# Kernel tuning notes

Hardware: AMD Instinct MI355X
Metric: run time of the kernel (lower is better)

Reference implementation:

```python
import jax, jax.numpy as jnp
import numpy as np

NEG_SLOPE = 0.2  # PyG GATConv default negative_slope


def _gat_layer(x, src, dst, n_nodes, W, a_src, a_dst, b):
    # x: [N, din]; src/dst: [E] (self-loops already included)
    h = x @ W                                  # [N, dout]
    s_src = h @ a_src                          # [N]
    s_dst = h @ a_dst                          # [N]
    e = jax.nn.leaky_relu(s_src[src] + s_dst[dst], NEG_SLOPE)  # [E]
    # per-target-node softmax over incoming edges (stable via segment max)
    m = jax.ops.segment_max(e, dst, num_segments=n_nodes)      # [N]
    a = jnp.exp(e - m[dst])                    # [E]
    denom = jax.ops.segment_sum(a, dst, num_segments=n_nodes)  # [N]
    msg = h[src] * a[:, None]                  # [E, dout]
    agg = jax.ops.segment_sum(msg, dst, num_segments=n_nodes)  # [N, dout]
    return agg / denom[:, None] + b


def setup_inputs() -> dict:
    key = jax.random.key(0)
    ks = jax.random.split(key, 16)
    N, E = 100000, 1600000
    in_dim, hid_dim, out_dim = 128, 128, 64
    x = jax.random.normal(ks[0], (N, in_dim), dtype=jnp.float32)
    edge_idx = jax.random.randint(ks[1], (2, E), 0, N, dtype=jnp.int32)

    def lin(k, din, dout):
        return jax.random.normal(k, (din, dout), dtype=jnp.float32) * (1.0 / np.sqrt(din))

    def att(k, dout):
        return jax.random.normal(k, (dout,), dtype=jnp.float32) * (1.0 / np.sqrt(dout))

    return {
        "x": x, "edge_idx": edge_idx,
        "W1": lin(ks[2], in_dim, hid_dim), "as1": att(ks[3], hid_dim), "ad1": att(ks[4], hid_dim), "b1": jnp.zeros((hid_dim,), jnp.float32),
        "W2": lin(ks[5], hid_dim, hid_dim), "as2": att(ks[6], hid_dim), "ad2": att(ks[7], hid_dim), "b2": jnp.zeros((hid_dim,), jnp.float32),
        "W3": lin(ks[8], hid_dim, out_dim), "as3": att(ks[9], out_dim), "ad3": att(ks[10], out_dim), "b3": jnp.zeros((out_dim,), jnp.float32),
    }


def reference(x, edge_idx, W1, as1, ad1, b1, W2, as2, ad2, b2, W3, as3, ad3, b3):
    N = x.shape[0]
    # add self-loops (PyG GATConv default add_self_loops=True)
    loops = jnp.arange(N, dtype=edge_idx.dtype)
    src = jnp.concatenate([edge_idx[0], loops])
    dst = jnp.concatenate([edge_idx[1], loops])
    h = _gat_layer(x, src, dst, N, W1, as1, ad1, b1)
    h = _gat_layer(h, src, dst, N, W2, as2, ad2, b2)
    h = _gat_layer(h, src, dst, N, W3, as3, ad3, b3)
    return jnp.mean(h, axis=-2)  # [out_dim]
```

## Files before the change

kernel.cpp:

```cpp
#include <hip/hip_runtime.h>

static inline int ceil_div(long long a, long long b) { return (int)((a + b - 1) / b); }

typedef __attribute__((ext_vector_type(8))) short bf16x8;
typedef __attribute__((ext_vector_type(4))) float f32x4;

__device__ __forceinline__ float lrelu(float t) { return t > 0.f ? t : 0.2f * t; }

__device__ __forceinline__ void atomAddF(float* p, float v) {
  unsafeAtomicAdd(p, v);
}

__device__ __forceinline__ unsigned int f2bf(float f) {
  unsigned int u = __float_as_uint(f);
  unsigned int r = ((u >> 16) & 1u) + 0x7fffu;
  return (u + r) >> 16;
}

__global__ void cvt_bf16(const float* __restrict__ X, unsigned short* __restrict__ Xb, int n4) {
  int i = blockIdx.x * blockDim.x + threadIdx.x;
  if (i < n4) {
    const float4 v = ((const float4*)X)[i];
    uint2 o;
    o.x = f2bf(v.x) | (f2bf(v.y) << 16);
    o.y = f2bf(v.z) | (f2bf(v.w) << 16);
    ((uint2*)Xb)[i] = o;
  }
}

__global__ void transpose_w(const float* __restrict__ W, unsigned short* __restrict__ Wt,
                            int DINv, int DOUTv) {
  int idx = blockIdx.x * blockDim.x + threadIdx.x;
  if (idx < DINv * DOUTv) {
    int k = idx / DOUTv, n = idx % DOUTv;
    Wt[n * DINv + k] = (unsigned short)f2bf(W[idx]);
  }
}

template<int DOUT>
__launch_bounds__(256)
__global__ void gemm_mfma(const unsigned short* __restrict__ Xb, const unsigned short* __restrict__ Wt,
                          const float* __restrict__ avs, const float* __restrict__ avd,
                          unsigned short* __restrict__ Hb, float* __restrict__ Ss,
                          float* __restrict__ Sd, int N, int RG) {
  constexpr int DIN = 128;
  constexpr int CG = DOUT / 64;
  const int wave = (int)((blockIdx.x * (unsigned)blockDim.x + threadIdx.x) >> 6);
  const int rg = wave / CG;
  const int cg = wave % CG;
  if (rg >= RG) return;
  const int lane = threadIdx.x & 63;
  const int l16 = lane & 15, quad = lane >> 4;
  const int row0 = rg * 64, colw0 = cg * 64;

  int xoff[4], woff[4];
#pragma unroll
  for (int t = 0; t < 4; t++) {
    int m = row0 + t * 16 + l16; if (m > N - 1) m = N - 1;
    xoff[t] = m * DIN + quad * 8;
    woff[t] = (colw0 + t * 16 + l16) * DIN + quad * 8;
  }

  f32x4 acc[4][4];
#pragma unroll
  for (int a = 0; a < 4; a++)
#pragma unroll
    for (int c = 0; c < 4; c++) acc[a][c] = (f32x4)0.f;

#pragma unroll
  for (int kk = 0; kk < 4; kk++) {
    bf16x8 aw[4], bx[4];
#pragma unroll
    for (int t = 0; t < 4; t++) aw[t] = *(const bf16x8*)(Wt + woff[t] + kk * 32);
#pragma unroll
    for (int t = 0; t < 4; t++) bx[t] = *(const bf16x8*)(Xb + xoff[t] + kk * 32);
#pragma unroll
    for (int wt = 0; wt < 4; wt++)
#pragma unroll
      for (int xt = 0; xt < 4; xt++)
        acc[wt][xt] = __builtin_amdgcn_mfma_f32_16x16x32_bf16(aw[wt], bx[xt], acc[wt][xt], 0, 0, 0);
  }

  float4 af[4], df[4];
#pragma unroll
  for (int wt = 0; wt < 4; wt++) {
    af[wt] = *(const float4*)(avs + colw0 + wt * 16 + quad * 4);
    df[wt] = *(const float4*)(avd + colw0 + wt * 16 + quad * 4);
  }
#pragma unroll
  for (int xt = 0; xt < 4; xt++) {
    const int m = row0 + xt * 16 + l16;
    float ps = 0.f, pd = 0.f;
#pragma unroll
    for (int wt = 0; wt < 4; wt++) {
      const f32x4 c = acc[wt][xt];
      ps += c[0]*af[wt].x + c[1]*af[wt].y + c[2]*af[wt].z + c[3]*af[wt].w;
      pd += c[0]*df[wt].x + c[1]*df[wt].y + c[2]*df[wt].z + c[3]*df[wt].w;
    }
    ps += __shfl_xor(ps, 16); ps += __shfl_xor(ps, 32);
    pd += __shfl_xor(pd, 16); pd += __shfl_xor(pd, 32);
    if (quad == 0 && m < N) { atomAddF(&Ss[m], ps); atomAddF(&Sd[m], pd); }
    if (m < N) {
      unsigned short* hp = Hb + (size_t)m * DOUT + colw0 + quad * 4;
#pragma unroll
      for (int wt = 0; wt < 4; wt++) {
        const f32x4 c = acc[wt][xt];
        uint2 o;
        o.x = f2bf(c[0]) | (f2bf(c[1]) << 16);
        o.y = f2bf(c[2]) | (f2bf(c[3]) << 16);
        *(uint2*)(hp + wt * 16) = o;
      }
    }
  }
}

__global__ void hist_rank(const int* __restrict__ dstv, int* __restrict__ cnt,
                          int* __restrict__ rank, int E) {
  int i = blockIdx.x * blockDim.x + threadIdx.x;
  if (i < E) rank[i] = atomicAdd(&cnt[dstv[i]], 1);
}

__global__ void scan_p1(const int* __restrict__ cnt, int* __restrict__ bsum, int N) {
  __shared__ int sm[256];
  const int b = blockIdx.x;
  int s = 0;
  for (int i = threadIdx.x; i < 1024; i += 256) {
    int idx = b * 1024 + i;
    s += (idx < N) ? cnt[idx] : 0;
  }
  sm[threadIdx.x] = s; __syncthreads();
  for (int off = 128; off; off >>= 1) {
    if (threadIdx.x < off) sm[threadIdx.x] += sm[threadIdx.x + off];
    __syncthreads();
  }
  if (threadIdx.x == 0) bsum[b] = sm[0];
}

__global__ void scan_p2(const int* __restrict__ bsum, int* __restrict__ bofs,
                        int NB, int* __restrict__ rowptr_N, int E) {
  __shared__ int sm[1024];
  const int t = threadIdx.x;
  const int v0 = (t < NB) ? bsum[t] : 0;
  sm[t] = v0; __syncthreads();
  for (int off = 1; off < 1024; off <<= 1) {
    int v = (t >= off) ? sm[t - off] : 0;
    __syncthreads();
    sm[t] += v;
    __syncthreads();
  }
  if (t < NB) bofs[t] = sm[t] - v0;
  if (t == 0) *rowptr_N = E;
}

__global__ void scan_p3(const int* __restrict__ cnt, const int* __restrict__ bofs,
                        int* __restrict__ rowptr, int N) {
  __shared__ int sm[1024];
  const int t = threadIdx.x;
  const int idx = blockIdx.x * 1024 + t;
  const int v = (idx < N) ? cnt[idx] : 0;
  sm[t] = v; __syncthreads();
  for (int off = 1; off < 1024; off <<= 1) {
    int u = (t >= off) ? sm[t - off] : 0;
    __syncthreads();
    sm[t] += u;
    __syncthreads();
  }
  if (idx < N) rowptr[idx] = sm[t] - v + bofs[blockIdx.x];
}

__global__ void scatter_k(const int* __restrict__ src, const int* __restrict__ dstv,
                          const int* __restrict__ rank, const int* __restrict__ rowptr,
                          int* __restrict__ srcs, int E) {
  int i = blockIdx.x * blockDim.x + threadIdx.x;
  if (i < E) srcs[rowptr[dstv[i]] + rank[i]] = src[i];
}

template<int DOUT, bool OBF>
__launch_bounds__(256)
__global__ void node_gather(const int* __restrict__ rowptr, const int* __restrict__ srcs,
                            const float* __restrict__ Ss, const float* __restrict__ Sd,
                            const unsigned short* __restrict__ Hb, const float* __restrict__ b,
                            float* __restrict__ out, unsigned short* __restrict__ outb, int N) {
  constexpr int EPL = DOUT / 16;
  constexpr int CAP = 64;
  __shared__ uint2 swL[16][CAP];

  const int l16 = threadIdx.x & 15;
  const int grp = threadIdx.x >> 4;
  const int node = blockIdx.x * 16 + grp;
  if (node >= N) return;

  const int r0 = rowptr[node], r1 = rowptr[node + 1];
  const int deg = r1 - r0;
  const int degc = min(deg, CAP);
  const float sd = Sd[node];
  const float eself = lrelu(Ss[node] + sd);

  float m = eself;
  for (int j0 = 0; j0 < deg; j0 += 16) {
    const int idx = j0 + l16;
    float e = -1e30f;
    if (idx < deg) {
      const int s = srcs[r0 + idx];
      e = lrelu(Ss[s] + sd);
      if (idx < CAP) swL[grp][idx] = make_uint2((unsigned)s, __float_as_uint(e));
    }
    m = fmaxf(m, e);
  }
#pragma unroll
  for (int off = 8; off; off >>= 1) m = fmaxf(m, __shfl_xor(m, off));

  const float wself = __expf(eself - m);
  float lsum = 0.f;
  for (int j0 = 0; j0 < degc; j0 += 16) {
    const int idx = j0 + l16;
    if (idx < degc) {
      uint2 sw = swL[grp][idx];
      const float w = __expf(__uint_as_float(sw.y) - m);
      sw.y = __float_as_uint(w);
      swL[grp][idx] = sw;
      lsum += w;
    }
  }
  for (int j0 = CAP; j0 < deg; j0 += 16) {
    const int idx = j0 + l16;
    if (idx < deg) {
      const int s = srcs[r0 + idx];
      lsum += __expf(lrelu(Ss[s] + sd) - m);
    }
  }
#pragma unroll
  for (int off = 8; off; off >>= 1) lsum += __shfl_xor(lsum, off);
  const float inv = 1.f / (lsum + wself);
  __syncthreads();

  float acc[EPL];
#pragma unroll
  for (int k = 0; k < EPL; k++) acc[k] = 0.f;

  const size_t colb = (size_t)l16 * EPL;
  int j = 0;
  for (; j + 4 <= degc; j += 4) {
    uint2 sw0 = swL[grp][j], sw1 = swL[grp][j+1], sw2 = swL[grp][j+2], sw3 = swL[grp][j+3];
    const unsigned short* p0 = Hb + (size_t)sw0.x * DOUT + colb;
    const unsigned short* p1 = Hb + (size_t)sw1.x * DOUT + colb;
    const unsigned short* p2 = Hb + (size_t)sw2.x * DOUT + colb;
    const unsigned short* p3 = Hb + (size_t)sw3.x * DOUT + colb;
    if (EPL == 8) {
      const uint4 u0 = *(const uint4*)p0, u1 = *(const uint4*)p1;
      const uint4 u2 = *(const uint4*)p2, u3 = *(const uint4*)p3;
      const float w0 = __uint_as_float(sw0.y), w1 = __uint_as_float(sw1.y);
      const float w2 = __uint_as_float(sw2.y), w3 = __uint_as_float(sw3.y);
      const unsigned int a0[4] = {u0.x,u0.y,u0.z,u0.w}, a1[4] = {u1.x,u1.y,u1.z,u1.w};
      const unsigned int a2[4] = {u2.x,u2.y,u2.z,u2.w}, a3[4] = {u3.x,u3.y,u3.z,u3.w};
#pragma unroll
      for (int k = 0; k < 4; k++) {
        acc[2*k]   += __uint_as_float(a0[k] << 16) * w0 + __uint_as_float(a1[k] << 16) * w1
                    + __uint_as_float(a2[k] << 16) * w2 + __uint_as_float(a3[k] << 16) * w3;
        acc[2*k+1] += __uint_as_float(a0[k] & 0xffff0000u) * w0 + __uint_as_float(a1[k] & 0xffff0000u) * w1
                    + __uint_as_float(a2[k] & 0xffff0000u) * w2 + __uint_as_float(a3[k] & 0xffff0000u) * w3;
      }
    } else {
      const uint2 u0 = *(const uint2*)p0, u1 = *(const uint2*)p1;
      const uint2 u2 = *(const uint2*)p2, u3 = *(const uint2*)p3;
      const float w0 = __uint_as_float(sw0.y), w1 = __uint_as_float(sw1.y);
      const float w2 = __uint_as_float(sw2.y), w3 = __uint_as_float(sw3.y);
      const unsigned int a0[2] = {u0.x,u0.y}, a1[2] = {u1.x,u1.y};
      const unsigned int a2[2] = {u2.x,u2.y}, a3[2] = {u3.x,u3.y};
#pragma unroll
      for (int k = 0; k < 2; k++) {
        acc[2*k]   += __uint_as_float(a0[k] << 16) * w0 + __uint_as_float(a1[k] << 16) * w1
                    + __uint_as_float(a2[k] << 16) * w2 + __uint_as_float(a3[k] << 16) * w3;
        acc[2*k+1] += __uint_as_float(a0[k] & 0xffff0000u) * w0 + __uint_as_float(a1[k] & 0xffff0000u) * w1
                    + __uint_as_float(a2[k] & 0xffff0000u) * w2 + __uint_as_float(a3[k] & 0xffff0000u) * w3;
      }
    }
  }
  for (; j < degc; j++) {
    const uint2 sw = swL[grp][j];
    const float w = __uint_as_float(sw.y);
    const unsigned short* pp = Hb + (size_t)sw.x * DOUT + colb;
#pragma unroll
    for (int k = 0; k < EPL / 2; k++) {
      const unsigned int u = ((const unsigned int*)pp)[k];
      acc[2*k]   += __uint_as_float(u << 16) * w;
      acc[2*k+1] += __uint_as_float(u & 0xffff0000u) * w;
    }
  }
  for (j = CAP; j < deg; j++) {
    const int s = srcs[r0 + j];
    const float w = __expf(lrelu(Ss[s] + sd) - m);
    const unsigned short* pp = Hb + (size_t)s * DOUT + colb;
#pragma unroll
    for (int k = 0; k < EPL / 2; k++) {
      const unsigned int u = ((const unsigned int*)pp)[k];
      acc[2*k]   += __uint_as_float(u << 16) * w;
      acc[2*k+1] += __uint_as_float(u & 0xffff0000u) * w;
    }
  }
  {
    const unsigned short* pp = Hb + (size_t)node * DOUT + colb;
#pragma unroll
    for (int k = 0; k < EPL / 2; k++) {
      const unsigned int u = ((const unsigned int*)pp)[k];
      acc[2*k]   += __uint_as_float(u << 16) * wself;
      acc[2*k+1] += __uint_as_float(u & 0xffff0000u) * wself;
    }
  }

  float o[EPL];
#pragma unroll
  for (int k = 0; k < EPL; k++) o[k] = acc[k] * inv + b[colb + k];
  if (OBF) {
    if (EPL == 8) {
      uint4 u;
      u.x = f2bf(o[0]) | (f2bf(o[1]) << 16);
      u.y = f2bf(o[2]) | (f2bf(o[3]) << 16);
      u.z = f2bf(o[4]) | (f2bf(o[5]) << 16);
      u.w = f2bf(o[6]) | (f2bf(o[7]) << 16);
      *(uint4*)(outb + (size_t)node * DOUT + colb) = u;
    } else {
      uint2 u;
      u.x = f2bf(o[0]) | (f2bf(o[1]) << 16);
      u.y = f2bf(o[2]) | (f2bf(o[3]) << 16);
      *(uint2*)(outb + (size_t)node * DOUT + colb) = u;
    }
  } else {
    float* op = out + (size_t)node * DOUT + colb;
#pragma unroll
    for (int k = 0; k < EPL; k += 4)
      *(float4*)(op + k) = make_float4(o[k], o[k+1], o[k+2], o[k+3]);
  }
}

__global__ void mean64(const float* __restrict__ Hf, float* __restrict__ out, int N, float scale) {
  __shared__ float sm[256];
  const int col = threadIdx.x & 63;
  const int seg = threadIdx.x >> 6;
  const int stride = gridDim.x * 4;
  float s = 0.f;
  for (int n = blockIdx.x * 4 + seg; n < N; n += stride) s += Hf[(size_t)n * 64 + col];
  sm[threadIdx.x] = s;
  __syncthreads();
  if (seg == 0) {
    float tot = sm[col] + sm[64 + col] + sm[128 + col] + sm[192 + col];
    atomAddF(&out[col], tot * scale);
  }
}

extern "C" void kernel_launch(void* const* d_in, const int* in_sizes, int n_in,
                              void* d_out, int out_size, void* d_ws, size_t ws_size,
                              hipStream_t stream) {
  const float* x   = (const float*)d_in[0];
  const int*   ei  = (const int*)d_in[1];
  const float* W1  = (const float*)d_in[2];
  const float* as1 = (const float*)d_in[3];
  const float* ad1 = (const float*)d_in[4];
  const float* b1  = (const float*)d_in[5];
  const float* W2  = (const float*)d_in[6];
  const float* as2 = (const float*)d_in[7];
  const float* ad2 = (const float*)d_in[8];
  const float* b2  = (const float*)d_in[9];
  const float* W3  = (const float*)d_in[10];
  const float* as3 = (const float*)d_in[11];
  const float* ad3 = (const float*)d_in[12];
  const float* b3  = (const float*)d_in[13];

  const int N = in_sizes[0] / 128;
  const int E = in_sizes[1] / 2;
  const int* src  = ei;
  const int* dstv = ei + E;
  const int NB = ceil_div(N, 1024);
  const int RG = ceil_div(N, 64);

  float* p = (float*)d_ws;
  float* bufA = p; p += (size_t)N * 64;
  float* SsSd = p; p += (size_t)2 * N;
  float* Ss = SsSd, *Sd = SsSd + N;
  unsigned short* Xb = (unsigned short*)p; p += (size_t)N * 64;
  unsigned short* Hb = (unsigned short*)p; p += (size_t)N * 64;
  unsigned short* Wt1 = (unsigned short*)p; p += 128 * 128 / 2;
  unsigned short* Wt2 = (unsigned short*)p; p += 128 * 128 / 2;
  unsigned short* Wt3 = (unsigned short*)p; p += 128 * 64 / 2;
  int* ip = (int*)p;
  int* cnt     = ip; ip += N;
  int* rowptr  = ip; ip += N + 1;
  int* bsum    = ip; ip += NB;
  int* bofs    = ip; ip += NB;
  int* rank    = ip; ip += E;
  int* srcs    = ip; ip += E;

  hipMemsetAsync(cnt, 0, (size_t)N * sizeof(int), stream);
  hist_rank<<<ceil_div(E, 256), 256, 0, stream>>>(dstv, cnt, rank, E);
  scan_p1<<<NB, 256, 0, stream>>>(cnt, bsum, N);
  scan_p2<<<1, 1024, 0, stream>>>(bsum, bofs, NB, rowptr + N, E);
  scan_p3<<<NB, 1024, 0, stream>>>(cnt, bofs, rowptr, N);
  scatter_k<<<ceil_div(E, 256), 256, 0, stream>>>(src, dstv, rank, rowptr, srcs, E);

  transpose_w<<<ceil_div(128 * 128, 256), 256, 0, stream>>>(W1, Wt1, 128, 128);
  transpose_w<<<ceil_div(128 * 128, 256), 256, 0, stream>>>(W2, Wt2, 128, 128);
  transpose_w<<<ceil_div(128 * 64, 256), 256, 0, stream>>>(W3, Wt3, 128, 64);
  cvt_bf16<<<ceil_div((long long)N * 32, 256), 256, 0, stream>>>(x, Xb, N * 32);

  const int GG = ceil_div(N, 16);
  hipMemsetAsync(SsSd, 0, (size_t)2 * N * sizeof(float), stream);
  gemm_mfma<128><<<ceil_div((long long)RG * 2, 4), 256, 0, stream>>>(Xb, Wt1, as1, ad1, Hb, Ss, Sd, N, RG);
  node_gather<128, true><<<GG, 256, 0, stream>>>(rowptr, srcs, Ss, Sd, Hb, b1, nullptr, Xb, N);
  hipMemsetAsync(SsSd, 0, (size_t)2 * N * sizeof(float), stream);
  gemm_mfma<128><<<ceil_div((long long)RG * 2, 4), 256, 0, stream>>>(Xb, Wt2, as2, ad2, Hb, Ss, Sd, N, RG);
  node_gather<128, true><<<GG, 256, 0, stream>>>(rowptr, srcs, Ss, Sd, Hb, b2, nullptr, Xb, N);
  hipMemsetAsync(SsSd, 0, (size_t)2 * N * sizeof(float), stream);
  gemm_mfma<64><<<ceil_div((long long)RG, 4), 256, 0, stream>>>(Xb, Wt3, as3, ad3, Hb, Ss, Sd, N, RG);
  node_gather<64, false><<<GG, 256, 0, stream>>>(rowptr, srcs, Ss, Sd, Hb, b3, bufA, nullptr, N);

  hipMemsetAsync(d_out, 0, 64 * sizeof(float), stream);
  mean64<<<256, 256, 0, stream>>>(bufA, (float*)d_out, N, 1.0f / (float)N);
}
```

Baseline: 488.2 us.

## Replace atomic CSR build with two-level bucketed counting sort

```diff
diff --git a/kernel.cpp b/kernel.cpp
--- a/kernel.cpp
+++ b/kernel.cpp
@@ -4,6 +4,9 @@
 
 typedef __attribute__((ext_vector_type(8))) short bf16x8;
 typedef __attribute__((ext_vector_type(4))) float f32x4;
+
+#define TILE 8192
+#define BKSH 9
 
 __device__ __forceinline__ float lrelu(float t) { return t > 0.f ? t : 0.2f * t; }
 
@@ -114,65 +117,103 @@
   }
 }
 
-__global__ void hist_rank(const int* __restrict__ dstv, int* __restrict__ cnt,
-                          int* __restrict__ rank, int E) {
-  int i = blockIdx.x * blockDim.x + threadIdx.x;
-  if (i < E) rank[i] = atomicAdd(&cnt[dstv[i]], 1);
-}
-
-__global__ void scan_p1(const int* __restrict__ cnt, int* __restrict__ bsum, int N) {
-  __shared__ int sm[256];
-  const int b = blockIdx.x;
+__launch_bounds__(256)
+__global__ void bucket_hist(const int* __restrict__ dstv, int* __restrict__ bh,
+                            int E, int NBUK) {
+  __shared__ int h[256];
+  h[threadIdx.x] = 0;
+  __syncthreads();
+  const int base = blockIdx.x * TILE;
+  const int end = min(E, base + TILE);
+  for (int i = base + threadIdx.x; i < end; i += 256)
+    atomicAdd(&h[dstv[i] >> BKSH], 1);
+  __syncthreads();
+  if (threadIdx.x < NBUK) bh[blockIdx.x * NBUK + threadIdx.x] = h[threadIdx.x];
+}
+
+__launch_bounds__(256)
+__global__ void bucket_scan(int* __restrict__ bh, int* __restrict__ bucketBase,
+                            int* __restrict__ rowptr_N, int NBA, int NBUK, int E) {
+  __shared__ int tot[256], sc[256];
+  const int t = threadIdx.x;
   int s = 0;
-  for (int i = threadIdx.x; i < 1024; i += 256) {
-    int idx = b * 1024 + i;
-    s += (idx < N) ? cnt[idx] : 0;
-  }
-  sm[threadIdx.x] = s; __syncthreads();
-  for (int off = 128; off; off >>= 1) {
-    if (threadIdx.x < off) sm[threadIdx.x] += sm[threadIdx.x + off];
+  if (t < NBUK)
+    for (int blk = 0; blk < NBA; blk++) s += bh[blk * NBUK + t];
+  tot[t] = s; sc[t] = s;
+  __syncthreads();
+  for (int off = 1; off < 256; off <<= 1) {
+    int v = (t >= off) ? sc[t - off] : 0;
     __syncthreads();
-  }
-  if (threadIdx.x == 0) bsum[b] = sm[0];
-}
-
-__global__ void scan_p2(const int* __restrict__ bsum, int* __restrict__ bofs,
-                        int NB, int* __restrict__ rowptr_N, int E) {
-  __shared__ int sm[1024];
+    sc[t] += v;
+    __syncthreads();
+  }
+  const int base = sc[t] - tot[t];
+  if (t < NBUK) bucketBase[t] = base;
+  if (t == 0) { bucketBase[NBUK] = E; *rowptr_N = E; }
+  if (t < NBUK) {
+    int run = base;
+    for (int blk = 0; blk < NBA; blk++) {
+      const int c = bh[blk * NBUK + t];
+      bh[blk * NBUK + t] = run;
+      run += c;
+    }
+  }
+}
+
+__launch_bounds__(256)
+__global__ void bucket_scatter(const int* __restrict__ src, const int* __restrict__ dstv,
+                               const int* __restrict__ bh, unsigned int* __restrict__ pairs,
+                               int E, int NBUK) {
+  __shared__ int ofs[256];
+  if (threadIdx.x < NBUK) ofs[threadIdx.x] = bh[blockIdx.x * NBUK + threadIdx.x];
+  __syncthreads();
+  const int base = blockIdx.x * TILE;
+  const int end = min(E, base + TILE);
+  for (int i = base + threadIdx.x; i < end; i += 256) {
+    const int d = dstv[i];
+    const int pos = atomicAdd(&ofs[d >> BKSH], 1);
+    pairs[pos] = ((unsigned int)src[i] << BKSH) | (unsigned int)(d & ((1 << BKSH) - 1));
+  }
+}
+
+__launch_bounds__(256)
+__global__ void region_build(const unsigned int* __restrict__ pairs,
+                             const int* __restrict__ bucketBase,
+                             int* __restrict__ rowptr, int* __restrict__ srcs, int N) {
+  __shared__ int cnt[512], ofs[512], ps[256];
   const int t = threadIdx.x;
-  const int v0 = (t < NB) ? bsum[t] : 0;
-  sm[t] = v0; __syncthreads();
-  for (int off = 1; off < 1024; off <<= 1) {
-    int v = (t >= off) ? sm[t - off] : 0;
+  const int r = blockIdx.x;
+  const int p0 = bucketBase[r], p1 = bucketBase[r + 1];
+  cnt[t] = 0; cnt[t + 256] = 0;
+  __syncthreads();
+  for (int i = p0 + t; i < p1; i += 256)
+    atomicAdd(&cnt[pairs[i] & 511u], 1);
+  __syncthreads();
+  const int c0 = cnt[2 * t], c1 = cnt[2 * t + 1];
+  const int pr = c0 + c1;
+  ps[t] = pr;
+  __syncthreads();
+  for (int off = 1; off < 256; off <<= 1) {
+    int v = (t >= off) ? ps[t - off] : 0;
     __syncthreads();
-    sm[t] += v;
+    ps[t] += v;
     __syncthreads();
   }
-  if (t < NB) bofs[t] = sm[t] - v0;
-  if (t == 0) *rowptr_N = E;
-}
-
-__global__ void scan_p3(const int* __restrict__ cnt, const int* __restrict__ bofs,
-                        int* __restrict__ rowptr, int N) {
-  __shared__ int sm[1024];
-  const int t = threadIdx.x;
-  const int idx = blockIdx.x * 1024 + t;
-  const int v = (idx < N) ? cnt[idx] : 0;
-  sm[t] = v; __syncthreads();
-  for (int off = 1; off < 1024; off <<= 1) {
-    int u = (t >= off) ? sm[t - off] : 0;
-    __syncthreads();
-    sm[t] += u;
-    __syncthreads();
-  }
-  if (idx < N) rowptr[idx] = sm[t] - v + bofs[blockIdx.x];
-}
-
-__global__ void scatter_k(const int* __restrict__ src, const int* __restrict__ dstv,
-                          const int* __restrict__ rank, const int* __restrict__ rowptr,
-                          int* __restrict__ srcs, int E) {
-  int i = blockIdx.x * blockDim.x + threadIdx.x;
-  if (i < E) srcs[rowptr[dstv[i]] + rank[i]] = src[i];
+  const int pbase = ps[t] - pr;
+  ofs[2 * t] = pbase; ofs[2 * t + 1] = pbase + c0;
+  __syncthreads();
+  {
+    const int d0 = (r << BKSH) + t;
+    if (d0 < N) rowptr[d0] = p0 + ofs[t];
+    const int d1 = (r << BKSH) + t + 256;
+    if (d1 < N) rowptr[d1] = p0 + ofs[t + 256];
+  }
+  __syncthreads();
+  for (int i = p0 + t; i < p1; i += 256) {
+    const unsigned int w = pairs[i];
+    const int pos = atomicAdd(&ofs[w & 511u], 1);
+    srcs[p0 + pos] = (int)(w >> BKSH);
+  }
 }
 
 template<int DOUT, bool OBF>
@@ -370,8 +411,9 @@
   const int E = in_sizes[1] / 2;
   const int* src  = ei;
   const int* dstv = ei + E;
-  const int NB = ceil_div(N, 1024);
   const int RG = ceil_div(N, 64);
+  const int NBA = ceil_div(E, TILE);
+  const int NBUK = ceil_div(N, 1 << BKSH);
 
   float* p = (float*)d_ws;
   float* bufA = p; p += (size_t)N * 64;
@@ -383,19 +425,16 @@
   unsigned short* Wt2 = (unsigned short*)p; p += 128 * 128 / 2;
   unsigned short* Wt3 = (unsigned short*)p; p += 128 * 64 / 2;
   int* ip = (int*)p;
-  int* cnt     = ip; ip += N;
-  int* rowptr  = ip; ip += N + 1;
-  int* bsum    = ip; ip += NB;
-  int* bofs    = ip; ip += NB;
-  int* rank    = ip; ip += E;
-  int* srcs    = ip; ip += E;
-
-  hipMemsetAsync(cnt, 0, (size_t)N * sizeof(int), stream);
-  hist_rank<<<ceil_div(E, 256), 256, 0, stream>>>(dstv, cnt, rank, E);
-  scan_p1<<<NB, 256, 0, stream>>>(cnt, bsum, N);
-  scan_p2<<<1, 1024, 0, stream>>>(bsum, bofs, NB, rowptr + N, E);
-  scan_p3<<<NB, 1024, 0, stream>>>(cnt, bofs, rowptr, N);
-  scatter_k<<<ceil_div(E, 256), 256, 0, stream>>>(src, dstv, rank, rowptr, srcs, E);
+  int* rowptr     = ip; ip += N + 1;
+  int* bh         = ip; ip += (size_t)NBA * NBUK;
+  int* bucketBase = ip; ip += NBUK + 1;
+  unsigned int* pairs = (unsigned int*)ip; ip += E;
+  int* srcs       = ip; ip += E;
+
+  bucket_hist<<<NBA, 256, 0, stream>>>(dstv, bh, E, NBUK);
+  bucket_scan<<<1, 256, 0, stream>>>(bh, bucketBase, rowptr + N, NBA, NBUK, E);
+  bucket_scatter<<<NBA, 256, 0, stream>>>(src, dstv, bh, pairs, E, NBUK);
+  region_build<<<NBUK, 256, 0, stream>>>(pairs, bucketBase, rowptr, srcs, N);
 
   transpose_w<<<ceil_div(128 * 128, 256), 256, 0, stream>>>(W1, Wt1, 128, 128);
   transpose_w<<<ceil_div(128 * 128, 256), 256, 0, stream>>>(W2, Wt2, 128, 128);
```

Measured after the change: 506.9 us. +3.8%, slower.
